# Optimization experiments

Measured on AMD Instinct MI355X. Metric: run time of the kernel, lower is better.

The kernel has to match this reference:

```python
import jax, jax.numpy as jnp
import numpy as np

B, N, M = 2, 2048, 2048
Q_DIM = 1024
HEADS = 8
DIM_HEAD = 64
INNER = HEADS * DIM_HEAD  # 512


def setup_inputs() -> dict:
    key = jax.random.key(0)
    ks = jax.random.split(key, 7)
    s_in = 1.0 / np.sqrt(Q_DIM)
    s_out = 1.0 / np.sqrt(INNER)
    return {
        "x": jax.random.normal(ks[0], (B, N, Q_DIM), dtype=jnp.float32),
        "context": jax.random.normal(ks[1], (B, M, Q_DIM), dtype=jnp.float32),
        "Wq": jax.random.normal(ks[2], (Q_DIM, INNER), dtype=jnp.float32) * s_in,
        "Wk": jax.random.normal(ks[3], (Q_DIM, INNER), dtype=jnp.float32) * s_in,
        "Wv": jax.random.normal(ks[4], (Q_DIM, INNER), dtype=jnp.float32) * s_in,
        "Wo": jax.random.normal(ks[5], (INNER, Q_DIM), dtype=jnp.float32) * s_out,
        "bo": jax.random.normal(ks[6], (Q_DIM,), dtype=jnp.float32) * 0.01,
    }


def reference(x, context, Wq, Wk, Wv, Wo, bo):
    scale = DIM_HEAD ** (-0.5)
    # projections, split heads: [b, n, inner] -> [b, h, n, d]
    def split_heads(t):
        b, n, _ = t.shape
        return t.reshape(b, n, HEADS, DIM_HEAD).transpose(0, 2, 1, 3)
    q = split_heads(x @ Wq)
    k = split_heads(context @ Wk)
    v = split_heads(context @ Wv)
    sim = jnp.einsum('bhid,bhjd->bhij', q, k) * scale  # [b,h,n,m] full score matrix
    attn = jax.nn.softmax(sim, axis=-1)
    out = jnp.einsum('bhij,bhjd->bhid', attn, v)       # [b,h,n,d]
    out = out.transpose(0, 2, 1, 3).reshape(x.shape[0], x.shape[1], INNER)
    return out @ Wo + bo
```

## Files before the change

kernel.cpp:

```cpp
#include <hip/hip_runtime.h>

typedef __attribute__((ext_vector_type(8))) short short8;
typedef __attribute__((ext_vector_type(4))) short bf16x4;
typedef __attribute__((ext_vector_type(4))) float floatx4;
typedef __attribute__((ext_vector_type(4))) float f32x4;

__device__ __forceinline__ short f2bf(float f) {
    union { float f; unsigned u; } v;
    v.f = f;
    unsigned r = v.u + 0x7fffu + ((v.u >> 16) & 1u);
    return (short)(r >> 16);
}
__device__ __forceinline__ short8 cvt8(f32x4 a, f32x4 b) {
    short8 r;
    r[0] = f2bf(a[0]); r[1] = f2bf(a[1]); r[2] = f2bf(a[2]); r[3] = f2bf(a[3]);
    r[4] = f2bf(b[0]); r[5] = f2bf(b[1]); r[6] = f2bf(b[2]); r[7] = f2bf(b[3]);
    return r;
}
__device__ __forceinline__ bf16x4 pack4(float a, float b, float c, float d) {
    union { float f; unsigned u; } x;
    unsigned ua, ub, uc, ud;
    x.f = a; ua = (x.u + 0x8000u) >> 16;
    x.f = b; ub = (x.u + 0x8000u) >> 16;
    x.f = c; uc = (x.u + 0x8000u) >> 16;
    x.f = d; ud = (x.u + 0x8000u) >> 16;
    union { bf16x4 s; unsigned u2[2]; } r;
    r.u2[0] = ua | (ub << 16);
    r.u2[1] = uc | (ud << 16);
    return r.s;
}

#define MFMA_BF16(a, b, c) __builtin_amdgcn_mfma_f32_16x16x32_bf16((a), (b), (c), 0, 0, 0)

__device__ __forceinline__ floatx4 mfma16(bf16x4 a, bf16x4 b, floatx4 c) {
#if __has_builtin(__builtin_amdgcn_mfma_f32_16x16x16bf16_1k)
    return __builtin_amdgcn_mfma_f32_16x16x16bf16_1k(a, b, c, 0, 0, 0);
#else
    floatx4 d;
    asm volatile("v_mfma_f32_16x16x16_bf16 %0, %1, %2, %3"
                 : "=&v"(d) : "v"(a), "v"(b), "v"(c));
    return d;
#endif
}

__device__ __forceinline__ float fast_exp2(float x) {
#if __has_builtin(__builtin_amdgcn_exp2f)
    return __builtin_amdgcn_exp2f(x);
#else
    return exp2f(x);
#endif
}

#define QSCALE_LOG2E 0.18033688011112042f

__global__ __launch_bounds__(256) void wfrag_all(const float* __restrict__ Wq,
                                                 const float* __restrict__ Wk,
                                                 const float* __restrict__ Wv,
                                                 const float* __restrict__ Wo,
                                                 short* __restrict__ WqF,
                                                 short* __restrict__ WkF,
                                                 short* __restrict__ WvF,
                                                 short* __restrict__ WoF) {
    const int z = blockIdx.y;
    const float* src = (z == 0) ? Wq : (z == 1) ? Wk : (z == 2) ? Wv : Wo;
    short* dst = (z == 0) ? WqF : (z == 1) ? WkF : (z == 2) ? WvF : WoF;
    const int nbits = (z < 3) ? 9 : 10;
    const int N = 1 << nbits;
    const int t = blockIdx.x * 256 + threadIdx.x;
    const int kb = t >> nbits;
    const int n = t & (N - 1);
    const float* s = src + (size_t)(kb * 8) * N + n;
    short8 v;
#pragma unroll
    for (int j = 0; j < 8; ++j) v[j] = f2bf(s[(size_t)j * N]);
    *(short8*)(dst + (size_t)t * 8) = v;
}

__global__ __launch_bounds__(256) void afrag(const float* __restrict__ x,
                                             const float* __restrict__ ctx,
                                             short* __restrict__ AxF,
                                             short* __restrict__ AcF) {
    const float* src = (blockIdx.z == 0) ? x : ctx;
    short* dst = (blockIdx.z == 0) ? AxF : AcF;
    const int r0 = blockIdx.x * 64;
    const int k0 = blockIdx.y * 64;
    __shared__ short tile[64][72];
    const int tid = threadIdx.x;
    {
        const int seg = tid & 15;
        const int rbase = tid >> 4;
#pragma unroll
        for (int i = 0; i < 4; ++i) {
            const int row = rbase + i * 16;
            f32x4 v = *(const f32x4*)(src + (size_t)(r0 + row) * 1024 + k0 + seg * 4);
#pragma unroll
            for (int jj = 0; jj < 4; ++jj) tile[row][seg * 4 + jj] = f2bf(v[jj]);
        }
    }
    __syncthreads();
    {
        const int kbl = tid >> 5;
        const int rbase = tid & 31;
#pragma unroll
        for (int j = 0; j < 2; ++j) {
            const int row = rbase + j * 32;
            short8 v = *(const short8*)(&tile[row][kbl * 8]);
            *(short8*)(dst + ((size_t)(k0 / 8 + kbl) * 4096 + r0 + row) * 8) = v;
        }
    }
}

__global__ __launch_bounds__(256, 4) void gemm_qkv(const short* __restrict__ AxF,
                                                   const short* __restrict__ AcF,
                                                   const short* __restrict__ WqF,
                                                   const short* __restrict__ WkF,
                                                   const short* __restrict__ WvF,
                                                   short* __restrict__ Qw,
                                                   short* __restrict__ Kw,
                                                   short* __restrict__ Vtw) {
    const int z = blockIdx.z;
    const short* AF = (z == 0) ? AxF : AcF;
    const short* WF = (z == 0) ? WqF : (z == 1) ? WkF : WvF;
    const int tid = threadIdx.x;
    const int w = tid >> 6;
    const int lane = tid & 63;
    const int quad = lane >> 4, ln = lane & 15;
    const int wr = w >> 1, wc = w & 1;
    const int row0 = blockIdx.x * 64;
    const int col0 = blockIdx.y * 128;

    const short* aBase = AF + ((size_t)quad * 4096 + row0 + wr * 32 + ln) * 8;
    const short* bBase = WF + ((size_t)quad * 512 + col0 + wc * 64 + ln) * 8;

    floatx4 acc[2][4] = {};
    short8 aR[3][2], bR[3][4];

    auto loadStep = [&](int it) {
        const int s = it % 3;
#pragma unroll
        for (int i = 0; i < 2; ++i)
            aR[s][i] = *(const short8*)(aBase + (size_t)it * 131072 + i * 128);
#pragma unroll
        for (int t = 0; t < 4; ++t)
            bR[s][t] = *(const short8*)(bBase + (size_t)it * 16384 + t * 128);
    };

    loadStep(0);
    loadStep(1);
#pragma unroll
    for (int it = 0; it < 32; ++it) {
        if (it + 2 < 32) loadStep(it + 2);
        const int s = it % 3;
#pragma unroll
        for (int i = 0; i < 2; ++i)
#pragma unroll
            for (int t = 0; t < 4; ++t)
                acc[i][t] = MFMA_BF16(aR[s][i], bR[s][t], acc[i][t]);
    }

    const float oscale = (z == 0) ? QSCALE_LOG2E : 1.0f;
    short* dst = (z == 0) ? Qw : (z == 1) ? Kw : Vtw;
#pragma unroll
    for (int i = 0; i < 2; ++i)
#pragma unroll
        for (int t = 0; t < 4; ++t)
#pragma unroll
            for (int r = 0; r < 4; ++r) {
                const int R = row0 + wr * 32 + i * 16 + quad * 4 + r;
                const int C = col0 + wc * 64 + t * 16 + ln;
                const int b = R >> 11, n = R & 2047;
                const int h = C >> 6, d = C & 63;
                const short val = f2bf(acc[i][t][r] * oscale);
                if (z < 2)
                    dst[((b * 8 + h) * 2048 + n) * 64 + d] = val;
                else
                    dst[((b * 8 + h) * 64 + d) * 2048 + n] = val;
            }
}

__global__ __launch_bounds__(256, 2) void attn_kernel(const short* __restrict__ Q,
                                                      const short* __restrict__ K,
                                                      const short* __restrict__ Vt,
                                                      short* __restrict__ AwF) {
    const int tid = threadIdx.x;
    const int w = tid >> 6;
    const int lane = tid & 63;
    const int quad = lane >> 4;
    const int ln = lane & 15;
    const int q0 = blockIdx.x * 64;
    const int bh = blockIdx.y;

    __shared__ __align__(16) short klds[2][64][72];
    __shared__ __align__(16) short vlds[2][64][72];

    const short* Qbh = Q + bh * 2048 * 64;
    const short* Kbh = K + bh * 2048 * 64;
    const short* Vbh = Vt + bh * 64 * 2048;

    short8 qf[2];
    {
        const int qrow = q0 + w * 16 + ln;
        qf[0] = *(const short8*)(Qbh + qrow * 64 + quad * 8);
        qf[1] = *(const short8*)(Qbh + qrow * 64 + 32 + quad * 8);
    }

    floatx4 ot[4] = {};
    float lp = 0.f;

    const int sr = tid >> 3;
    const int sc = (tid & 7) * 8;

    auto computeTile = [&](int b) {
        short8 kf[8];
#pragma unroll
        for (int t = 0; t < 4; ++t)
#pragma unroll
            for (int ks = 0; ks < 2; ++ks)
                kf[t * 2 + ks] = *(const short8*)(&klds[b][t * 16 + ln][ks * 32 + quad * 8]);
        bf16x4 vf[16];
#pragma unroll
        for (int dt = 0; dt < 4; ++dt)
#pragma unroll
            for (int t = 0; t < 4; ++t)
                vf[dt * 4 + t] = *(const bf16x4*)(&vlds[b][dt * 16 + ln][t * 16 + quad * 4]);

        floatx4 s[4] = {};
#pragma unroll
        for (int ks = 0; ks < 2; ++ks)
#pragma unroll
            for (int t = 0; t < 4; ++t)
                s[t] = MFMA_BF16(kf[t * 2 + ks], qf[ks], s[t]);

        bf16x4 pf[4];
#pragma unroll
        for (int t = 0; t < 4; ++t) {
            float p0 = fast_exp2(s[t][0]);
            float p1 = fast_exp2(s[t][1]);
            float p2 = fast_exp2(s[t][2]);
            float p3 = fast_exp2(s[t][3]);
            lp += (p0 + p1) + (p2 + p3);
            pf[t] = pack4(p0, p1, p2, p3);
        }
#pragma unroll
        for (int t = 0; t < 4; ++t)
#pragma unroll
            for (int dt = 0; dt < 4; ++dt)
                ot[dt] = mfma16(vf[dt * 4 + t], pf[t], ot[dt]);
    };

    const int nt = 2048 / 64;

    {
        short8 k0 = *(const short8*)(Kbh + tid * 8);
        short8 k1 = *(const short8*)(Kbh + (tid + 256) * 8);
        short8 v0 = *(const short8*)(Vbh + sr * 2048 + sc);
        short8 v1 = *(const short8*)(Vbh + (sr + 32) * 2048 + sc);
        *(short8*)(&klds[0][sr][sc]) = k0;
        *(short8*)(&klds[0][sr + 32][sc]) = k1;
        *(short8*)(&vlds[0][sr][sc]) = v0;
        *(short8*)(&vlds[0][sr + 32][sc]) = v1;
    }
    __syncthreads();

    for (int it = 0; it < nt; ++it) {
        short8 k0, k1, v0, v1;
        const bool more = (it + 1 < nt);
        if (more) {
            const int jn = (it + 1) * 64;
            k0 = *(const short8*)(Kbh + jn * 64 + tid * 8);
            k1 = *(const short8*)(Kbh + jn * 64 + (tid + 256) * 8);
            v0 = *(const short8*)(Vbh + sr * 2048 + jn + sc);
            v1 = *(const short8*)(Vbh + (sr + 32) * 2048 + jn + sc);
        }
        computeTile(it & 1);
        if (more) {
            const int nb = (it + 1) & 1;
            *(short8*)(&klds[nb][sr][sc]) = k0;
            *(short8*)(&klds[nb][sr + 32][sc]) = k1;
            *(short8*)(&vlds[nb][sr][sc]) = v0;
            *(short8*)(&vlds[nb][sr + 32][sc]) = v1;
        }
        __syncthreads();
    }

    lp += __shfl_xor(lp, 16);
    lp += __shfl_xor(lp, 32);
    const float invL = 1.0f / lp;

    const int n = q0 + w * 16 + ln;
    const int b = bh >> 3, h = bh & 7;
    const int R = b * 2048 + n;
#pragma unroll
    for (int dt = 0; dt < 4; ++dt) {
        const int kb = h * 8 + dt * 2 + (quad >> 1);
        short* p = AwF + ((size_t)kb * 4096 + R) * 8 + (quad & 1) * 4;
        *(bf16x4*)p = pack4(ot[dt][0] * invL, ot[dt][1] * invL,
                            ot[dt][2] * invL, ot[dt][3] * invL);
    }
}

__global__ __launch_bounds__(256, 4) void gemm_final(const short* __restrict__ AwF,
                                                     const short* __restrict__ WoF,
                                                     const float* __restrict__ bias,
                                                     float* __restrict__ out) {
    const int tid = threadIdx.x;
    const int w = tid >> 6;
    const int lane = tid & 63;
    const int quad = lane >> 4, ln = lane & 15;
    const int wr = w >> 1, wc = w & 1;
    const int row0 = blockIdx.x * 64;
    const int col0 = blockIdx.y * 128;

    const short* aBase = AwF + ((size_t)quad * 4096 + row0 + wr * 32 + ln) * 8;
    const short* bBase = WoF + ((size_t)quad * 1024 + col0 + wc * 64 + ln) * 8;

    floatx4 acc[2][4] = {};
    short8 aR[3][2], bR[3][4];

    auto loadStep = [&](int it) {
        const int s = it % 3;
#pragma unroll
        for (int i = 0; i < 2; ++i)
            aR[s][i] = *(const short8*)(aBase + (size_t)it * 131072 + i * 128);
#pragma unroll
        for (int t = 0; t < 4; ++t)
            bR[s][t] = *(const short8*)(bBase + (size_t)it * 32768 + t * 128);
    };

    loadStep(0);
    loadStep(1);
#pragma unroll
    for (int it = 0; it < 16; ++it) {
        if (it + 2 < 16) loadStep(it + 2);
        const int s = it % 3;
#pragma unroll
        for (int i = 0; i < 2; ++i)
#pragma unroll
            for (int t = 0; t < 4; ++t)
                acc[i][t] = MFMA_BF16(aR[s][i], bR[s][t], acc[i][t]);
    }

#pragma unroll
    for (int i = 0; i < 2; ++i)
#pragma unroll
        for (int t = 0; t < 4; ++t)
#pragma unroll
            for (int r = 0; r < 4; ++r) {
                const int R = row0 + wr * 32 + i * 16 + quad * 4 + r;
                const int C = col0 + wc * 64 + t * 16 + ln;
                out[(size_t)R * 1024 + C] = acc[i][t][r] + bias[C];
            }
}

extern "C" void kernel_launch(void* const* d_in, const int* in_sizes, int n_in,
                              void* d_out, int out_size, void* d_ws, size_t ws_size,
                              hipStream_t stream) {
    const float* x   = (const float*)d_in[0];
    const float* ctx = (const float*)d_in[1];
    const float* Wq  = (const float*)d_in[2];
    const float* Wk  = (const float*)d_in[3];
    const float* Wv  = (const float*)d_in[4];
    const float* Wo  = (const float*)d_in[5];
    const float* bo  = (const float*)d_in[6];
    float* out = (float*)d_out;

    char* ws = (char*)d_ws;
    size_t off = 0;
    auto alloc = [&](size_t bytes) { char* p = ws + off; off += (bytes + 255) & ~(size_t)255; return p; };

    short* WqF  = (short*)alloc(512 * 1024 * 2);
    short* WkF  = (short*)alloc(512 * 1024 * 2);
    short* WvF  = (short*)alloc(512 * 1024 * 2);
    short* WoF  = (short*)alloc(1024 * 512 * 2);
    short* AxF  = (short*)alloc((size_t)4096 * 1024 * 2);
    short* AcF  = (short*)alloc((size_t)4096 * 1024 * 2);
    short* Qw   = (short*)alloc((size_t)16 * 2048 * 64 * 2);
    short* Kw   = (short*)alloc((size_t)16 * 2048 * 64 * 2);
    short* Vtw  = (short*)alloc((size_t)16 * 2048 * 64 * 2);
    short* AwF  = (short*)alloc((size_t)4096 * 512 * 2);

    wfrag_all<<<dim3(256, 4), 256, 0, stream>>>(Wq, Wk, Wv, Wo, WqF, WkF, WvF, WoF);
    afrag<<<dim3(64, 16, 2), 256, 0, stream>>>(x, ctx, AxF, AcF);

    gemm_qkv<<<dim3(64, 4, 3), 256, 0, stream>>>(AxF, AcF, WqF, WkF, WvF, Qw, Kw, Vtw);

    attn_kernel<<<dim3(32, 16), 256, 0, stream>>>(Qw, Kw, Vtw, AwF);

    gemm_final<<<dim3(64, 8), 256, 0, stream>>>(AwF, WoF, bo, out);
}
```

Baseline: 167.5 us.

## Restructure attention kernel with 32x32 MFMA, KV-split waves and direct LDS loads

Rewrites the attention kernel so each wave processes a disjoint quarter of the key/value tiles for all 64 queries, using 32x32x16 bf16 MFMA, and reduces the partial outputs and denominators across waves through shared memory at the end. K/V tiles are staged with global_load_lds into swizzled per-wave LDS buffers, P is packed with v_cvt_pk_bf16 and permlane32 swaps, and blocks are remapped so each XCD handles two heads. The aim is fewer MFMA issues, no register round-trip for LDS staging, better L2 locality, and higher matrix-core utilisation. In exchange it adds a cross-wave reduction epilogue, uses 64KB LDS per block, and relies on gfx950-specific instructions.

```diff
diff --git a/kernel.cpp b/kernel.cpp
--- a/kernel.cpp
+++ b/kernel.cpp
@@ -1,8 +1,8 @@
 #include <hip/hip_runtime.h>
 
 typedef __attribute__((ext_vector_type(8))) short short8;
-typedef __attribute__((ext_vector_type(4))) short bf16x4;
 typedef __attribute__((ext_vector_type(4))) float floatx4;
+typedef __attribute__((ext_vector_type(16))) float f32x16;
 typedef __attribute__((ext_vector_type(4))) float f32x4;
 
 __device__ __forceinline__ short f2bf(float f) {
@@ -11,37 +11,9 @@
     unsigned r = v.u + 0x7fffu + ((v.u >> 16) & 1u);
     return (short)(r >> 16);
 }
-__device__ __forceinline__ short8 cvt8(f32x4 a, f32x4 b) {
-    short8 r;
-    r[0] = f2bf(a[0]); r[1] = f2bf(a[1]); r[2] = f2bf(a[2]); r[3] = f2bf(a[3]);
-    r[4] = f2bf(b[0]); r[5] = f2bf(b[1]); r[6] = f2bf(b[2]); r[7] = f2bf(b[3]);
-    return r;
-}
-__device__ __forceinline__ bf16x4 pack4(float a, float b, float c, float d) {
-    union { float f; unsigned u; } x;
-    unsigned ua, ub, uc, ud;
-    x.f = a; ua = (x.u + 0x8000u) >> 16;
-    x.f = b; ub = (x.u + 0x8000u) >> 16;
-    x.f = c; uc = (x.u + 0x8000u) >> 16;
-    x.f = d; ud = (x.u + 0x8000u) >> 16;
-    union { bf16x4 s; unsigned u2[2]; } r;
-    r.u2[0] = ua | (ub << 16);
-    r.u2[1] = uc | (ud << 16);
-    return r.s;
-}
 
 #define MFMA_BF16(a, b, c) __builtin_amdgcn_mfma_f32_16x16x32_bf16((a), (b), (c), 0, 0, 0)
-
-__device__ __forceinline__ floatx4 mfma16(bf16x4 a, bf16x4 b, floatx4 c) {
-#if __has_builtin(__builtin_amdgcn_mfma_f32_16x16x16bf16_1k)
-    return __builtin_amdgcn_mfma_f32_16x16x16bf16_1k(a, b, c, 0, 0, 0);
-#else
-    floatx4 d;
-    asm volatile("v_mfma_f32_16x16x16_bf16 %0, %1, %2, %3"
-                 : "=&v"(d) : "v"(a), "v"(b), "v"(c));
-    return d;
-#endif
-}
+#define MFMA32(a, b, c)    __builtin_amdgcn_mfma_f32_32x32x16_bf16((a), (b), (c), 0, 0, 0)
 
 __device__ __forceinline__ float fast_exp2(float x) {
 #if __has_builtin(__builtin_amdgcn_exp2f)
@@ -49,6 +21,22 @@
 #else
     return exp2f(x);
 #endif
+}
+
+__device__ __forceinline__ unsigned cvtpk(float lo, float hi) {
+    unsigned r;
+    asm("v_cvt_pk_bf16_f32 %0, %1, %2" : "=v"(r) : "v"(lo), "v"(hi));
+    return r;
+}
+
+__device__ __forceinline__ void pl32(unsigned& a, unsigned& b) {
+    asm("v_permlane32_swap_b32 %0, %1" : "+v"(a), "+v"(b));
+}
+
+__device__ __forceinline__ void gll16(const void* g, void* l) {
+    __builtin_amdgcn_global_load_lds((const __attribute__((address_space(1))) void*)g,
+                                     (__attribute__((address_space(3))) void*)l,
+                                     16, 0, 0);
 }
 
 #define QSCALE_LOG2E 0.18033688011112042f
@@ -185,117 +173,164 @@
     const int tid = threadIdx.x;
     const int w = tid >> 6;
     const int lane = tid & 63;
-    const int quad = lane >> 4;
-    const int ln = lane & 15;
-    const int q0 = blockIdx.x * 64;
-    const int bh = blockIdx.y;
-
-    __shared__ __align__(16) short klds[2][64][72];
-    __shared__ __align__(16) short vlds[2][64][72];
-
-    const short* Qbh = Q + bh * 2048 * 64;
-    const short* Kbh = K + bh * 2048 * 64;
-    const short* Vbh = Vt + bh * 64 * 2048;
-
-    short8 qf[2];
+    const int hi = lane >> 5;
+    const int ln5 = lane & 31;
+
+    const int L = blockIdx.x + 32 * blockIdx.y;
+    const int xcd = L & 7, slot = L >> 3;
+    const int bh = xcd * 2 + (slot >> 5);
+    const int q0 = (slot & 31) * 64;
+
+    __shared__ __align__(16) char smem[65536];
+    char* const wbase = smem + w * 16384;
+
+    const short* Qbh = Q + (size_t)bh * 2048 * 64;
+    const char* kp = (const char*)(K + (size_t)bh * 2048 * 64);
+    const char* vp = (const char*)(Vt + (size_t)bh * 64 * 2048);
+
+    short8 qf[2][4];
+#pragma unroll
+    for (int qt = 0; qt < 2; ++qt)
+#pragma unroll
+        for (int ds = 0; ds < 4; ++ds)
+            qf[qt][ds] = *(const short8*)(Qbh + (size_t)(q0 + qt * 32 + ln5) * 64 + ds * 16 + hi * 8);
+
+    f32x16 O[2][2] = {};
+    float lp0 = 0.f, lp1 = 0.f;
+
+    const int lrow = lane >> 3, lu = lane & 7;
+    const int swzK = ((lu ^ lrow) << 4);
+    const int sw_r = (ln5 & 7) << 4;
+
+    auto stageK = [&](int tile, int c) {
+        char* kb = wbase + c * 8192;
+#pragma unroll
+        for (int i = 0; i < 4; ++i)
+            gll16(kp + (size_t)tile * 4096 + (size_t)i * 1024 + lrow * 128 + swzK,
+                  kb + i * 1024);
+    };
+    auto stageV = [&](int tile, int c) {
+        char* vb = wbase + c * 8192 + 4096;
+#pragma unroll
+        for (int i = 0; i < 4; ++i) {
+            const int u = lu ^ lrow;
+            const int d = i * 8 + lrow + 32 * (u >> 2);
+            gll16(vp + (size_t)d * 4096 + (size_t)tile * 64 + (u & 3) * 16,
+                  vb + i * 1024);
+        }
+    };
+
+    short8 PA[2][2];
+
+    auto computeTile = [&](int c) {
+        char* kb = wbase + c * 8192;
+        char* vb = kb + 4096;
+        short8 kf[4];
+#pragma unroll
+        for (int ds = 0; ds < 4; ++ds)
+            kf[ds] = *(const short8*)(kb + ln5 * 128 + ((((ds * 2 + hi) << 4)) ^ sw_r));
+        f32x16 s0 = {}, s1 = {};
+        __builtin_amdgcn_s_setprio(1);
+#pragma unroll
+        for (int ds = 0; ds < 4; ++ds) {
+            s0 = MFMA32(kf[ds], qf[0][ds], s0);
+            s1 = MFMA32(kf[ds], qf[1][ds], s1);
+        }
+        __builtin_amdgcn_s_setprio(0);
+        auto buildPA = [&](const f32x16& sv, float& lacc, short8& oA, short8& oB) {
+            float p[16];
+#pragma unroll
+            for (int e = 0; e < 16; ++e) p[e] = fast_exp2(sv[e]);
+            float t0 = 0.f, t1 = 0.f;
+#pragma unroll
+            for (int e = 0; e < 16; e += 2) { t0 += p[e]; t1 += p[e + 1]; }
+            lacc += t0 + t1;
+            unsigned c0 = cvtpk(p[0], p[1]),   c1 = cvtpk(p[2], p[3]);
+            unsigned c2 = cvtpk(p[4], p[5]),   c3 = cvtpk(p[6], p[7]);
+            unsigned c4 = cvtpk(p[8], p[9]),   c5 = cvtpk(p[10], p[11]);
+            unsigned c6 = cvtpk(p[12], p[13]), c7 = cvtpk(p[14], p[15]);
+            pl32(c0, c2); pl32(c1, c3);
+            pl32(c4, c6); pl32(c5, c7);
+            union U { short8 s8; unsigned u[4]; };
+            U a; a.u[0] = c0; a.u[1] = c1; a.u[2] = c2; a.u[3] = c3; oA = a.s8;
+            U b; b.u[0] = c4; b.u[1] = c5; b.u[2] = c6; b.u[3] = c7; oB = b.s8;
+        };
+        buildPA(s0, lp0, PA[0][0], PA[1][0]);
+        buildPA(s1, lp1, PA[0][1], PA[1][1]);
+        short8 vf[2][2];
+#pragma unroll
+        for (int dt = 0; dt < 2; ++dt)
+#pragma unroll
+            for (int k2 = 0; k2 < 2; ++k2)
+                vf[dt][k2] = *(const short8*)(vb + ln5 * 128 +
+                                              ((((dt * 4 + k2 * 2 + hi) << 4)) ^ sw_r));
+        __builtin_amdgcn_s_setprio(1);
+#pragma unroll
+        for (int dt = 0; dt < 2; ++dt)
+#pragma unroll
+            for (int k2 = 0; k2 < 2; ++k2) {
+                O[dt][0] = MFMA32(vf[dt][k2], PA[k2][0], O[dt][0]);
+                O[dt][1] = MFMA32(vf[dt][k2], PA[k2][1], O[dt][1]);
+            }
+        __builtin_amdgcn_s_setprio(0);
+    };
+
+    stageK(w, 0);
+    stageV(w, 0);
+    __syncthreads();
+    int cur = 0;
+    for (int t = 0; t < 16; ++t) {
+        if (t < 15) {
+            stageK(w + (t + 1) * 4, cur ^ 1);
+            stageV(w + (t + 1) * 4, cur ^ 1);
+        }
+        computeTile(cur);
+        __syncthreads();
+        cur ^= 1;
+    }
+
+    float* lpf = (float*)smem;
     {
-        const int qrow = q0 + w * 16 + ln;
-        qf[0] = *(const short8*)(Qbh + qrow * 64 + quad * 8);
-        qf[1] = *(const short8*)(Qbh + qrow * 64 + 32 + quad * 8);
-    }
-
-    floatx4 ot[4] = {};
-    float lp = 0.f;
-
-    const int sr = tid >> 3;
-    const int sc = (tid & 7) * 8;
-
-    auto computeTile = [&](int b) {
-        short8 kf[8];
-#pragma unroll
-        for (int t = 0; t < 4; ++t)
-#pragma unroll
-            for (int ks = 0; ks < 2; ++ks)
-                kf[t * 2 + ks] = *(const short8*)(&klds[b][t * 16 + ln][ks * 32 + quad * 8]);
-        bf16x4 vf[16];
-#pragma unroll
-        for (int dt = 0; dt < 4; ++dt)
-#pragma unroll
-            for (int t = 0; t < 4; ++t)
-                vf[dt * 4 + t] = *(const bf16x4*)(&vlds[b][dt * 16 + ln][t * 16 + quad * 4]);
-
-        floatx4 s[4] = {};
-#pragma unroll
-        for (int ks = 0; ks < 2; ++ks)
-#pragma unroll
-            for (int t = 0; t < 4; ++t)
-                s[t] = MFMA_BF16(kf[t * 2 + ks], qf[ks], s[t]);
-
-        bf16x4 pf[4];
-#pragma unroll
-        for (int t = 0; t < 4; ++t) {
-            float p0 = fast_exp2(s[t][0]);
-            float p1 = fast_exp2(s[t][1]);
-            float p2 = fast_exp2(s[t][2]);
-            float p3 = fast_exp2(s[t][3]);
-            lp += (p0 + p1) + (p2 + p3);
-            pf[t] = pack4(p0, p1, p2, p3);
-        }
-#pragma unroll
-        for (int t = 0; t < 4; ++t)
-#pragma unroll
-            for (int dt = 0; dt < 4; ++dt)
-                ot[dt] = mfma16(vf[dt * 4 + t], pf[t], ot[dt]);
-    };
-
-    const int nt = 2048 / 64;
-
-    {
-        short8 k0 = *(const short8*)(Kbh + tid * 8);
-        short8 k1 = *(const short8*)(Kbh + (tid + 256) * 8);
-        short8 v0 = *(const short8*)(Vbh + sr * 2048 + sc);
-        short8 v1 = *(const short8*)(Vbh + (sr + 32) * 2048 + sc);
-        *(short8*)(&klds[0][sr][sc]) = k0;
-        *(short8*)(&klds[0][sr + 32][sc]) = k1;
-        *(short8*)(&vlds[0][sr][sc]) = v0;
-        *(short8*)(&vlds[0][sr + 32][sc]) = v1;
+        const float a = lp0 + __shfl_xor(lp0, 32);
+        const float b = lp1 + __shfl_xor(lp1, 32);
+        if (hi == 0) {
+            lpf[w * 64 + ln5] = a;
+            lpf[w * 64 + 32 + ln5] = b;
+        }
     }
     __syncthreads();
-
-    for (int it = 0; it < nt; ++it) {
-        short8 k0, k1, v0, v1;
-        const bool more = (it + 1 < nt);
-        if (more) {
-            const int jn = (it + 1) * 64;
-            k0 = *(const short8*)(Kbh + jn * 64 + tid * 8);
-            k1 = *(const short8*)(Kbh + jn * 64 + (tid + 256) * 8);
-            v0 = *(const short8*)(Vbh + sr * 2048 + jn + sc);
-            v1 = *(const short8*)(Vbh + (sr + 32) * 2048 + jn + sc);
-        }
-        computeTile(it & 1);
-        if (more) {
-            const int nb = (it + 1) & 1;
-            *(short8*)(&klds[nb][sr][sc]) = k0;
-            *(short8*)(&klds[nb][sr + 32][sc]) = k1;
-            *(short8*)(&vlds[nb][sr][sc]) = v0;
-            *(short8*)(&vlds[nb][sr + 32][sc]) = v1;
-        }
-        __syncthreads();
-    }
-
-    lp += __shfl_xor(lp, 16);
-    lp += __shfl_xor(lp, 32);
-    const float invL = 1.0f / lp;
-
-    const int n = q0 + w * 16 + ln;
+    const int qq = tid & 63;
+    const int k8a = tid >> 6;
+    const float den = lpf[qq] + lpf[64 + qq] + lpf[128 + qq] + lpf[192 + qq];
+    const float inv = 1.0f / den;
+    __syncthreads();
+    float* freg = (float*)smem + w * 4096;
+#pragma unroll
+    for (int dt = 0; dt < 2; ++dt)
+#pragma unroll
+        for (int qt = 0; qt < 2; ++qt)
+#pragma unroll
+            for (int e = 0; e < 16; ++e) {
+                const int d = dt * 32 + (e & 3) + 8 * (e >> 2) + 4 * hi;
+                freg[d * 64 + qt * 32 + ln5] = O[dt][qt][e];
+            }
+    __syncthreads();
     const int b = bh >> 3, h = bh & 7;
-    const int R = b * 2048 + n;
-#pragma unroll
-    for (int dt = 0; dt < 4; ++dt) {
-        const int kb = h * 8 + dt * 2 + (quad >> 1);
-        short* p = AwF + ((size_t)kb * 4096 + R) * 8 + (quad & 1) * 4;
-        *(bf16x4*)p = pack4(ot[dt][0] * invL, ot[dt][1] * invL,
-                            ot[dt][2] * invL, ot[dt][3] * invL);
+    const float* fall = (const float*)smem;
+#pragma unroll
+    for (int j = 0; j < 2; ++j) {
+        const int k8 = k8a + j * 4;
+        float a8[8];
+#pragma unroll
+        for (int dd = 0; dd < 8; ++dd) {
+            const int d = k8 * 8 + dd;
+            a8[dd] = fall[d * 64 + qq] + fall[4096 + d * 64 + qq] +
+                     fall[8192 + d * 64 + qq] + fall[12288 + d * 64 + qq];
+        }
+        short8 o8;
+#pragma unroll
+        for (int dd = 0; dd < 8; ++dd) o8[dd] = f2bf(a8[dd] * inv);
+        *(short8*)(AwF + ((size_t)(h * 8 + k8) * 4096 + (size_t)(b * 2048 + q0 + qq)) * 8) = o8;
     }
 }
 
```

Result: faster. 157.1 us (-6.2%).
